# Kernel optimization log

Measured on AMD Instinct MI355X. Metric: run time of the kernel, lower is better.

The kernel has to match this reference:

```python
import jax, jax.numpy as jnp
import numpy as np

NEIGHBOUR_NUM = 8  # args.neighbour_num


def _sqrdis_map(x, y):
    # x: [B,M,3], y: [B,N,3] -> [B,M,N] squared distances
    x2 = jnp.sum(x * x, axis=-1)
    y2 = jnp.sum(y * y, axis=-1)
    inner = jnp.einsum('bmd,bnd->bmn', x, y)
    return x2[:, :, None] + y2[:, None, :] - 2.0 * inner


def _chamfer(x, y):
    d = _sqrdis_map(x, y)
    return d.min(axis=2), d.min(axis=1)


def _neighbor_index(v, k):
    # torch.topk(dist, k+1, largest=False) then drop self
    d = _sqrdis_map(v, v)
    idx = jax.lax.top_k(-d, k + 1)[1]  # ascending distance order
    return idx[:, :, 1:]


def _arap(idx, dp, sp):
    B = dp.shape[0]
    bid = jnp.arange(B)[:, None, None]
    dn = dp[bid, idx] - dp[:, :, None, :]  # [B,N,K,3]
    sn = sp[bid, idx] - sp[:, :, None, :]
    dd = jnp.sqrt(jnp.sum(dn * dn, axis=-1) + 1e-5)
    sd = jnp.sqrt(jnp.sum(sn * sn, axis=-1) + 1e-5)
    diff = dd - sd
    return jnp.sum(diff * diff) / B


def setup_inputs() -> dict:
    key = jax.random.key(0)
    ks = jax.random.split(key, 7)
    T, B, N = 3, 4, 4096
    return {
        'phi': jax.random.normal(ks[0], (T, B, 1024), dtype=jnp.float32),
        'point_weight': jax.random.normal(ks[1], (T, B, N, 1), dtype=jnp.float32),
        'deform_rigid_points': 0.5 * jax.random.normal(ks[2], (T, B, N, 3), dtype=jnp.float32),
        'deformation_points': 0.5 * jax.random.normal(ks[3], (T, B, N, 3), dtype=jnp.float32),
        'rigid_matrix': 0.1 * jax.random.normal(ks[4], (T, B, 4, 4), dtype=jnp.float32),
        'source_points': jax.random.uniform(ks[5], (B, N, 3), dtype=jnp.float32, minval=-1.0, maxval=1.0),
        'target_points': jax.random.uniform(ks[6], (B, N, 3), dtype=jnp.float32, minval=-1.0, maxval=1.0),
    }


def reference(phi, point_weight, deform_rigid_points, deformation_points,
              rigid_matrix, source_points, target_points):
    B = source_points.shape[0]
    T = phi.shape[0]  # iter_time = len(phi_list)
    idx = _neighbor_index(source_points, NEIGHBOUR_NUM)
    trans_mask = jnp.zeros((4, 4), dtype=rigid_matrix.dtype).at[0:3, 3].set(1.0)
    total = jnp.asarray(0.0, dtype=source_points.dtype)
    for t in range(T):  # small fixed iter count, structurally distinct stages
        dp = deformation_points[t]
        # loss_on_cd
        d1, d2 = _chamfer(dp, target_points)
        cd = (jnp.sum(d1) + jnp.sum(d2)) * 0.5 / B
        # loss_on_pd (rigid-deformed vs full deformation)
        diff = deform_rigid_points[t] - dp
        pd = jnp.sum(diff * diff) / B
        # loss_on_sparse
        sp = jnp.mean(jnp.abs(point_weight[t]))
        # loss_on_tran
        tr = trans_mask[None] * rigid_matrix[t]
        tran = jnp.sum(tr * tr) / B
        # loss_on_arap
        ar = _arap(idx, dp, source_points)
        total = total + cd + pd + sp + tran + ar
    return total
```

## Files before the change

### kernel.cpp

```cpp
#include <hip/hip_runtime.h>

#define T_ 3
#define B_ 4
#define N_ 4096
#define K_ 8

#define GROUPS 32
#define GRP_KNN 32
#define GRP_CH  12
#define GRP_SZ  45
#define CWIN 512

typedef short bf16x8 __attribute__((ext_vector_type(8)));
typedef float f32x4  __attribute__((ext_vector_type(4)));
typedef float f32x16 __attribute__((ext_vector_type(16)));

template <int NW>
__device__ inline float block_reduce(float v, float* scratch) {
    #pragma unroll
    for (int off = 32; off > 0; off >>= 1) v += __shfl_down(v, off, 64);
    const int lane = threadIdx.x & 63, wid = threadIdx.x >> 6;
    if (lane == 0) scratch[wid] = v;
    __syncthreads();
    float s = 0.f;
    if (threadIdx.x == 0) {
        #pragma unroll
        for (int w = 0; w < NW; ++w) s += scratch[w];
    }
    return s;
}

#define CE_(A, i, j) { unsigned lo_ = min(A[i], A[j]); A[j] = max(A[i], A[j]); A[i] = lo_; }
__device__ inline void sort8(unsigned s[8]) {
    CE_(s,0,1) CE_(s,2,3) CE_(s,4,5) CE_(s,6,7)
    CE_(s,0,2) CE_(s,1,3) CE_(s,4,6) CE_(s,5,7)
    CE_(s,1,2) CE_(s,5,6)
    CE_(s,0,4) CE_(s,1,5) CE_(s,2,6) CE_(s,3,7)
    CE_(s,2,4) CE_(s,3,5)
    CE_(s,1,2) CE_(s,3,4) CE_(s,5,6)
}
__device__ inline void merge_top8(unsigned a[8], const unsigned s[8]) {
    #pragma unroll
    for (int i = 0; i < 8; ++i) a[i] = min(a[i], s[7 - i]);
    CE_(a,0,4) CE_(a,1,5) CE_(a,2,6) CE_(a,3,7)
    CE_(a,0,2) CE_(a,1,3) CE_(a,4,6) CE_(a,5,7)
    CE_(a,0,1) CE_(a,2,3) CE_(a,4,5) CE_(a,6,7)
}

__device__ inline short hi16(float v) { return (short)(__float_as_uint(v) >> 16); }
__device__ inline float residual(float v) {
    return v - __uint_as_float(__float_as_uint(v) & 0xFFFF0000u);
}
__device__ inline unsigned pk2(short a, short b) {
    return (unsigned)(unsigned short)a | ((unsigned)(unsigned short)b << 16);
}
#define BF16_ONE ((short)0x3F80)

__global__ __launch_bounds__(256, 6) void mega_kernel(const float* __restrict__ src,
                                                      const float* __restrict__ dp_all,
                                                      const float* __restrict__ tp,
                                                      const float* __restrict__ drp,
                                                      const float* __restrict__ pw,
                                                      const float* __restrict__ rm,
                                                      float* __restrict__ out) {
    __shared__ uint4 smem4[1024];
    const f32x4 zero4 = {0.f, 0.f, 0.f, 0.f};

    const int g = blockIdx.x / GRP_SZ;
    const int r = blockIdx.x % GRP_SZ;

    if (r < GRP_KNN) {
        const int knn_id = g * GRP_KNN + r;
        uint4* alds = smem4;
        const int b   = knn_id / (N_ / 16);
        const int qt0 = (knn_id % (N_ / 16)) * 16;
        const float* sb = src + (size_t)b * N_ * 3;

        const int wid  = __builtin_amdgcn_readfirstlane(threadIdx.x >> 6);
        const int lane = threadIdx.x & 63;
        const int n    = lane & 15;
        const int quad = lane >> 4;
        const int rbase = quad * 4;
        const int qid  = qt0 + n;

        bf16x8 bfrag = (bf16x8)(short)0;
        {
            float x = sb[3 * qid], y = sb[3 * qid + 1], z = sb[3 * qid + 2];
            float q2 = fmaf(x, x, fmaf(y, y, z * z));
            short hx = hi16(x), hy = hi16(y), hz = hi16(z);
            short lx = hi16(residual(x)), ly = hi16(residual(y)), lz = hi16(residual(z));
            if (quad == 0) bfrag = (bf16x8){hx, hy, hz, hx, hy, hz, BF16_ONE, BF16_ONE};
            else if (quad == 1) bfrag = (bf16x8){lx, ly, lz, lx, ly, lz,
                                                 hi16(q2), hi16(residual(q2))};
        }

        unsigned a[K_];
        #pragma unroll
        for (int p = 0; p < K_; ++p) a[p] = 0xFFFFFFFFu;

        for (int w = 0; w < N_ / CWIN; ++w) {
            __syncthreads();
            #pragma unroll
            for (int rr = 0; rr < 2; ++rr) {
                int jloc = rr * 256 + threadIdx.x;
                int jg = w * CWIN + jloc;
                float x = sb[3 * jg], y = sb[3 * jg + 1], z = sb[3 * jg + 2];
                float p2 = fmaf(x, x, fmaf(y, y, z * z));
                float mx = -2.f * x, my = -2.f * y, mz = -2.f * z;
                short mhx = hi16(mx), mhy = hi16(my), mhz = hi16(mz);
                short mlx = hi16(residual(mx)), mly = hi16(residual(my)), mlz = hi16(residual(mz));
                uint4 f0 = make_uint4(pk2(mhx, mhy), pk2(mhz, mlx), pk2(mly, mlz),
                                      pk2(hi16(p2), hi16(residual(p2))));
                uint4 f1 = make_uint4(f0.x, f0.y, f0.z, pk2(BF16_ONE, BF16_ONE));
                int tile = jloc >> 4, m = jloc & 15;
                alds[tile * 32 + m]      = f0;
                alds[tile * 32 + 16 + m] = f1;
            }
            __syncthreads();

            #pragma unroll
            for (int bt = 0; bt < 4; ++bt) {
                unsigned s8[8];
                #pragma unroll
                for (int h = 0; h < 2; ++h) {
                    const int tile = wid * 8 + bt * 2 + h;
                    const int tbg  = w * CWIN + tile * 16;
                    bf16x8 af = (bf16x8)(short)0;
                    if (quad < 2) {
                        union { uint4 u; bf16x8 v; } cv;
                        cv.u = alds[tile * 32 + quad * 16 + n];
                        af = cv.v;
                    }
                    f32x4 d = __builtin_amdgcn_mfma_f32_16x16x32_bf16(af, bfrag, zero4, 0, 0, 0);
                    #pragma unroll
                    for (int rr = 0; rr < 4; ++rr)
                        s8[h * 4 + rr] = (__float_as_uint(d[rr]) & 0xFFFFF000u)
                                         | (unsigned)(tbg | (rbase + rr));
                    if (tbg == qt0) {
                        #pragma unroll
                        for (int rr = 0; rr < 4; ++rr)
                            if (rbase + rr == n) s8[h * 4 + rr] = 0xFFFFFFFFu;
                    }
                }
                sort8(s8);
                merge_top8(a, s8);
            }
        }

        #pragma unroll
        for (int mk = 16; mk <= 32; mk <<= 1) {
            unsigned t[8];
            #pragma unroll
            for (int e = 0; e < K_; ++e) t[e] = __shfl_xor(a[e], mk, 64);
            merge_top8(a, t);
        }

        __syncthreads();
        unsigned* sm = (unsigned*)smem4;
        unsigned* nidx = (unsigned*)smem4 + 1024;
        if (lane < 16) {
            #pragma unroll
            for (int e = 0; e < K_; ++e) sm[(wid * 16 + n) * 9 + e] = a[e];
        }
        __syncthreads();
        if (threadIdx.x < 16) {
            const int q = threadIdx.x;
            unsigned md[K_];
            #pragma unroll
            for (int e = 0; e < K_; ++e) md[e] = sm[q * 9 + e];
            #pragma unroll
            for (int wv = 1; wv < 4; ++wv) {
                unsigned t[8];
                #pragma unroll
                for (int e = 0; e < K_; ++e) t[e] = sm[(wv * 16 + q) * 9 + e];
                merge_top8(md, t);
            }
            #pragma unroll
            for (int e = 0; e < K_; ++e) nidx[q * 8 + e] = md[e] & 0xFFFu;
        }
        __syncthreads();

        float acc = 0.f;
        if (threadIdx.x < 16 * K_) {
            const int q  = threadIdx.x >> 3;
            const int qi = qt0 + q;
            const int j  = (int)nidx[threadIdx.x];
            float sx = sb[3 * qi], sy = sb[3 * qi + 1], sz = sb[3 * qi + 2];
            float ex = sb[3 * j] - sx, ey = sb[3 * j + 1] - sy, ez = sb[3 * j + 2] - sz;
            float sd = sqrtf(fmaf(ex, ex, fmaf(ey, ey, ez * ez)) + 1e-5f);
            #pragma unroll
            for (int t = 0; t < T_; ++t) {
                const float* dpb = dp_all + ((size_t)(t * B_ + b)) * N_ * 3;
                float dx = dpb[3 * j] - dpb[3 * qi];
                float dy = dpb[3 * j + 1] - dpb[3 * qi + 1];
                float dz = dpb[3 * j + 2] - dpb[3 * qi + 2];
                float dd = sqrtf(fmaf(dx, dx, fmaf(dy, dy, dz * dz)) + 1e-5f);
                float df = dd - sd;
                acc = fmaf(df, df, acc);
            }
        }
        float s = block_reduce<4>(acc, (float*)smem4);
        if (threadIdx.x == 0) atomicAdd(out, s * (1.0f / B_));

    } else if (r < GRP_KNN + GRP_CH) {
        const f32x16 zero16 = {0.f,0.f,0.f,0.f, 0.f,0.f,0.f,0.f,
                               0.f,0.f,0.f,0.f, 0.f,0.f,0.f,0.f};
        uint4* alds = smem4;
        const int cb = g * GRP_CH + (r - GRP_KNN);
        const int tbd  = cb >> 4;
        const int slab = cb & 15;
        const int dir = tbd & 1;
        const int tb  = tbd >> 1;
        const int b = tb % B_, t = tb / B_;

        const float* dpb = dp_all + ((size_t)(t * B_ + b)) * N_ * 3;
        const float* tpb = tp + (size_t)b * N_ * 3;
        const float* cbase = dir ? dpb : tpb;
        const float* qbase = dir ? tpb : dpb;

        const int lane = threadIdx.x & 63;
        const int wid  = __builtin_amdgcn_readfirstlane(threadIdx.x >> 6);
        const int col  = lane & 31;
        const int kg   = lane >> 5;

        bf16x8 bfrag[2];
        #pragma unroll
        for (int s = 0; s < 2; ++s) {
            const int qid = slab * 256 + s * 128 + wid * 32 + col;
            float x = qbase[3 * qid], y = qbase[3 * qid + 1], z = qbase[3 * qid + 2];
            float q2 = fmaf(x, x, fmaf(y, y, z * z));
            short hx = hi16(x), hy = hi16(y), hz = hi16(z);
            short lx = hi16(residual(x)), ly = hi16(residual(y)), lz = hi16(residual(z));
            if (kg == 0) bfrag[s] = (bf16x8){hx, hy, hz, hx, hy, hz, lx, ly};
            else bfrag[s] = (bf16x8){lz, lx, ly, lz, BF16_ONE, BF16_ONE,
                                     hi16(q2), hi16(residual(q2))};
        }

        float run0 = 3.4e38f, run1 = 3.4e38f;

        for (int w = 0; w < N_ / CWIN; ++w) {
            __syncthreads();
            #pragma unroll
            for (int rr = 0; rr < 2; ++rr) {
                int j = rr * 256 + (int)threadIdx.x;
                int jg = w * CWIN + j;
                float x = cbase[3 * jg], y = cbase[3 * jg + 1], z = cbase[3 * jg + 2];
                float p2 = fmaf(x, x, fmaf(y, y, z * z));
                float mx = -2.f * x, my = -2.f * y, mz = -2.f * z;
                short mhx = hi16(mx), mhy = hi16(my), mhz = hi16(mz);
                short mlx = hi16(residual(mx)), mly = hi16(residual(my)), mlz = hi16(residual(mz));
                unsigned w0 = pk2(mhx, mhy), w1 = pk2(mhz, mlx), w2 = pk2(mly, mlz);
                unsigned pw2 = pk2(hi16(p2), hi16(residual(p2)));
                alds[j]       = make_uint4(w0, w1, w2, w0);
                alds[512 + j] = make_uint4(w1, w2, pw2, pk2(BF16_ONE, BF16_ONE));
            }
            __syncthreads();

            #pragma unroll
            for (int tile = 0; tile < CWIN / 32; ++tile) {
                union { uint4 u; bf16x8 v; } cv;
                cv.u = alds[kg * 512 + tile * 32 + col];
                {
                    f32x16 d = __builtin_amdgcn_mfma_f32_32x32x16_bf16(cv.v, bfrag[0], zero16, 0, 0, 0);
                    float m0 = fminf(fminf(d[0],  d[1]),  fminf(d[2],  d[3]));
                    float m1 = fminf(fminf(d[4],  d[5]),  fminf(d[6],  d[7]));
                    float m2 = fminf(fminf(d[8],  d[9]),  fminf(d[10], d[11]));
                    float m3 = fminf(fminf(d[12], d[13]), fminf(d[14], d[15]));
                    run0 = fminf(run0, fminf(fminf(m0, m1), fminf(m2, m3)));
                }
                {
                    f32x16 d = __builtin_amdgcn_mfma_f32_32x32x16_bf16(cv.v, bfrag[1], zero16, 0, 0, 0);
                    float m0 = fminf(fminf(d[0],  d[1]),  fminf(d[2],  d[3]));
                    float m1 = fminf(fminf(d[4],  d[5]),  fminf(d[6],  d[7]));
                    float m2 = fminf(fminf(d[8],  d[9]),  fminf(d[10], d[11]));
                    float m3 = fminf(fminf(d[12], d[13]), fminf(d[14], d[15]));
                    run1 = fminf(run1, fminf(fminf(m0, m1), fminf(m2, m3)));
                }
            }
        }

        run0 = fminf(run0, __shfl_xor(run0, 32, 64));
        run1 = fminf(run1, __shfl_xor(run1, 32, 64));
        float vsum = (lane < 32) ? (run0 + run1) : 0.f;
        __syncthreads();
        float ssum = block_reduce<4>(vsum, (float*)smem4);
        if (threadIdx.x == 0) atomicAdd(out, ssum * (0.5f / B_));

    } else {
        const int PD_N = T_ * B_ * N_ * 3;
        const int SP_N = T_ * B_ * N_;
        const int stride = GROUPS * 256;
        const int gid = g * 256 + threadIdx.x;
        float apd = 0.f;
        for (int i = gid; i < PD_N; i += stride) {
            float d = drp[i] - dp_all[i];
            apd = fmaf(d, d, apd);
        }
        float asp = 0.f;
        for (int i = gid; i < SP_N; i += stride) asp += fabsf(pw[i]);
        float atr = 0.f;
        if (gid < T_ * B_ * 3) {
            int t = gid / (B_ * 3);
            int b = (gid / 3) % B_;
            int rr = gid % 3;
            float v = rm[t * B_ * 16 + b * 16 + rr * 4 + 3];
            atr = v * v;
        }
        float acc = apd * (1.0f / B_) + asp * (1.0f / (B_ * N_)) + atr * (1.0f / B_);
        float s = block_reduce<4>(acc, (float*)smem4);
        if (threadIdx.x == 0) atomicAdd(out, s);
    }
}

extern "C" void kernel_launch(void* const* d_in, const int* in_sizes, int n_in,
                              void* d_out, int out_size, void* d_ws, size_t ws_size,
                              hipStream_t stream) {
    const float* pw  = (const float*)d_in[1];
    const float* drp = (const float*)d_in[2];
    const float* dp  = (const float*)d_in[3];
    const float* rm  = (const float*)d_in[4];
    const float* sp  = (const float*)d_in[5];
    const float* tp  = (const float*)d_in[6];
    float* out = (float*)d_out;

    hipMemsetAsync(out, 0, sizeof(float), stream);
    mega_kernel<<<GROUPS * GRP_SZ, 256, 0, stream>>>(sp, dp, tp, drp, pw, rm, out);
}
```

Measured before the change: 121.9 us.

## Prefetch next point window into LDS with async global-to-LDS loads

The KNN and chamfer paths now read each window's raw xyz coordinates from a 6 KB LDS staging buffer. That buffer is filled with global_load_lds DMA, and the load for window w+1 is issued right after the barrier, so it overlaps the MFMA and sort work on window w. The aim is to take global-load latency off the critical path of the per-window conversion step. In exchange, each block uses more LDS, and correctness depends on the barrier waiting for the async vmcnt loads to finish.

```diff
diff --git a/kernel.cpp b/kernel.cpp
--- a/kernel.cpp
+++ b/kernel.cpp
@@ -56,6 +56,13 @@
 }
 #define BF16_ONE ((short)0x3F80)
 
+__device__ inline void async_ld(const float* g, float* l) {
+    __builtin_amdgcn_global_load_lds(
+        (const __attribute__((address_space(1))) void*)g,
+        (__attribute__((address_space(3))) void*)l,
+        4, 0, 0);
+}
+
 __global__ __launch_bounds__(256, 6) void mega_kernel(const float* __restrict__ src,
                                                       const float* __restrict__ dp_all,
                                                       const float* __restrict__ tp,
@@ -64,6 +71,7 @@
                                                       const float* __restrict__ rm,
                                                       float* __restrict__ out) {
     __shared__ uint4 smem4[1024];
+    __shared__ float raw[CWIN * 3];
     const f32x4 zero4 = {0.f, 0.f, 0.f, 0.f};
 
     const int g = blockIdx.x / GRP_SZ;
@@ -98,13 +106,18 @@
         #pragma unroll
         for (int p = 0; p < K_; ++p) a[p] = 0xFFFFFFFFu;
 
+        #pragma unroll
+        for (int c = 0; c < 6; ++c) {
+            const int chunk = c * 4 + wid;
+            async_ld(sb + chunk * 64 + lane, raw + chunk * 64);
+        }
+
         for (int w = 0; w < N_ / CWIN; ++w) {
             __syncthreads();
             #pragma unroll
             for (int rr = 0; rr < 2; ++rr) {
                 int jloc = rr * 256 + threadIdx.x;
-                int jg = w * CWIN + jloc;
-                float x = sb[3 * jg], y = sb[3 * jg + 1], z = sb[3 * jg + 2];
+                float x = raw[3 * jloc], y = raw[3 * jloc + 1], z = raw[3 * jloc + 2];
                 float p2 = fmaf(x, x, fmaf(y, y, z * z));
                 float mx = -2.f * x, my = -2.f * y, mz = -2.f * z;
                 short mhx = hi16(mx), mhy = hi16(my), mhz = hi16(mz);
@@ -117,6 +130,15 @@
                 alds[tile * 32 + 16 + m] = f1;
             }
             __syncthreads();
+
+            if (w + 1 < N_ / CWIN) {
+                const float* nb = sb + (w + 1) * (CWIN * 3);
+                #pragma unroll
+                for (int c = 0; c < 6; ++c) {
+                    const int chunk = c * 4 + wid;
+                    async_ld(nb + chunk * 64 + lane, raw + chunk * 64);
+                }
+            }
 
             #pragma unroll
             for (int bt = 0; bt < 4; ++bt) {
@@ -238,13 +260,18 @@
 
         float run0 = 3.4e38f, run1 = 3.4e38f;
 
+        #pragma unroll
+        for (int c = 0; c < 6; ++c) {
+            const int chunk = c * 4 + wid;
+            async_ld(cbase + chunk * 64 + lane, raw + chunk * 64);
+        }
+
         for (int w = 0; w < N_ / CWIN; ++w) {
             __syncthreads();
             #pragma unroll
             for (int rr = 0; rr < 2; ++rr) {
                 int j = rr * 256 + (int)threadIdx.x;
-                int jg = w * CWIN + j;
-                float x = cbase[3 * jg], y = cbase[3 * jg + 1], z = cbase[3 * jg + 2];
+                float x = raw[3 * j], y = raw[3 * j + 1], z = raw[3 * j + 2];
                 float p2 = fmaf(x, x, fmaf(y, y, z * z));
                 float mx = -2.f * x, my = -2.f * y, mz = -2.f * z;
                 short mhx = hi16(mx), mhy = hi16(my), mhz = hi16(mz);
@@ -255,6 +282,15 @@
                 alds[512 + j] = make_uint4(w1, w2, pw2, pk2(BF16_ONE, BF16_ONE));
             }
             __syncthreads();
+
+            if (w + 1 < N_ / CWIN) {
+                const float* nb = cbase + (w + 1) * (CWIN * 3);
+                #pragma unroll
+                for (int c = 0; c < 6; ++c) {
+                    const int chunk = c * 4 + wid;
+                    async_ld(nb + chunk * 64 + lane, raw + chunk * 64);
+                }
+            }
 
             #pragma unroll
             for (int tile = 0; tile < CWIN / 32; ++tile) {
```

Result: faster. 118.4 us (-2.9%).
